# Kernel optimization log

Hardware: AMD Instinct MI355X
Metric: run time of the kernel (lower is better)

The kernel has to match this reference:

```python
import jax, jax.numpy as jnp
import numpy as np

H = 32  # d_model
EPS = 1e-5  # LayerNorm eps (PyTorch default)


def _lstm_layer(x, W_ih, W_hh, b_ih, b_hh):
    """Single LSTM layer, batch_first x: (B, T, D) -> ys: (B, T, H).
    PyTorch gate order: i, f, g, o."""
    B, T, _ = x.shape
    # Hoist the input projection out of the recurrence: one big GEMM.
    xg = jnp.einsum('btd,gd->btg', x, W_ih) + b_ih + b_hh  # (B, T, 4H)
    xg = jnp.swapaxes(xg, 0, 1)  # (T, B, 4H) for scan over time

    def step(carry, xg_t):
        h, c = carry
        gates = xg_t + h @ W_hh.T  # (B, 4H)
        i, f, g, o = jnp.split(gates, 4, axis=-1)
        i = jax.nn.sigmoid(i)
        f = jax.nn.sigmoid(f)
        g = jnp.tanh(g)
        o = jax.nn.sigmoid(o)
        c = f * c + i * g
        h = o * jnp.tanh(c)
        return (h, c), h

    h0 = jnp.zeros((B, H), dtype=x.dtype)
    c0 = jnp.zeros((B, H), dtype=x.dtype)
    (_, _), ys = jax.lax.scan(step, (h0, c0), xg)
    return jnp.swapaxes(ys, 0, 1)  # (B, T, H)


def setup_inputs() -> dict:
    key = jax.random.key(0)
    ks = jax.random.split(key, 10)
    B, T, D = 4096, 512, 6
    s = 1.0 / np.sqrt(H)  # PyTorch LSTM init scale
    inp = {
        'x': jax.random.normal(ks[0], (B, T, D), dtype=jnp.float32),
        # layer 0: input_dim=6 -> H
        'W_ih0': jax.random.uniform(ks[1], (4 * H, D), minval=-s, maxval=s, dtype=jnp.float32),
        'W_hh0': jax.random.uniform(ks[2], (4 * H, H), minval=-s, maxval=s, dtype=jnp.float32),
        'b_ih0': jax.random.uniform(ks[3], (4 * H,), minval=-s, maxval=s, dtype=jnp.float32),
        'b_hh0': jax.random.uniform(ks[4], (4 * H,), minval=-s, maxval=s, dtype=jnp.float32),
        # layer 1: H -> H
        'W_ih1': jax.random.uniform(ks[5], (4 * H, H), minval=-s, maxval=s, dtype=jnp.float32),
        'W_hh1': jax.random.uniform(ks[6], (4 * H, H), minval=-s, maxval=s, dtype=jnp.float32),
        'b_ih1': jax.random.uniform(ks[7], (4 * H,), minval=-s, maxval=s, dtype=jnp.float32),
        'b_hh1': jax.random.uniform(ks[8], (4 * H,), minval=-s, maxval=s, dtype=jnp.float32),
        # final LayerNorm params
        'ln_gamma': jnp.ones((H,), dtype=jnp.float32),
        'ln_beta': jnp.zeros((H,), dtype=jnp.float32),
    }
    return inp


def reference(x, W_ih0, W_hh0, b_ih0, b_hh0, W_ih1, W_hh1, b_ih1, b_hh1, ln_gamma, ln_beta):
    # Two-layer LSTM (dropout between layers is a no-op in eval mode).
    h1 = _lstm_layer(x, W_ih0, W_hh0, b_ih0, b_hh0)   # (B, T, H)
    h2 = _lstm_layer(h1, W_ih1, W_hh1, b_ih1, b_hh1)  # (B, T, H)
    last = h2[:, -1, :]  # (B, H)
    mu = jnp.mean(last, axis=-1, keepdims=True)
    var = jnp.var(last, axis=-1, keepdims=True)
    return (last - mu) / jnp.sqrt(var + EPS) * ln_gamma + ln_beta
```

## Files before the change

kernel.cpp:

```cpp
#include <hip/hip_runtime.h>

#define TT   512
#define DD   6
#define HD   32
#define CH   32
#define EPSL 1e-5f
#define L2E  1.44269504f
#define L2E2 2.88539008f

typedef _Float16 half8 __attribute__((ext_vector_type(8)));
typedef __attribute__((ext_vector_type(4))) float f32x4;

#define MFMA_F16(a, b, c) __builtin_amdgcn_mfma_f32_16x16x32_f16((a), (b), (c), 0, 0, 0)

__global__ __launch_bounds__(256, 1) void lstm2_pipe(
    const float* __restrict__ x,
    const float* __restrict__ W_ih0,
    const float* __restrict__ W_hh0,
    const float* __restrict__ b_ih0,
    const float* __restrict__ b_hh0,
    const float* __restrict__ W_ih1,
    const float* __restrict__ W_hh1,
    const float* __restrict__ b_ih1,
    const float* __restrict__ b_hh1,
    const float* __restrict__ gamma,
    const float* __restrict__ beta,
    float* __restrict__ out)
{
    const int tid = threadIdx.x;
    const int w   = tid >> 6;
    const int L   = w >> 1;
    const int uh  = w & 1;
    const int ln  = tid & 63;
    const int q   = ln >> 4;
    const int n   = ln & 15;
    const int u   = 16 * uh + n;
    const int b0  = blockIdx.x << 4;

    __shared__ __align__(16) _Float16 h0r[4][16][40];
    __shared__ __align__(16) _Float16 h1r[2][16][40];
    __shared__ __align__(16) _Float16 xs[2][CH][16][8];
    __shared__ float ln_s[16][33];

    {
        unsigned* p0 = (unsigned*)&h0r[0][0][0];
        for (int i = tid; i < (int)(sizeof(h0r) / 4); i += 256) p0[i] = 0u;
        unsigned* p1 = (unsigned*)&h1r[0][0][0];
        for (int i = tid; i < (int)(sizeof(h1r) / 4); i += 256) p1[i] = 0u;
        unsigned* p2 = (unsigned*)&xs[0][0][0][0];
        for (int i = tid; i < (int)(sizeof(xs) / 4); i += 256) p2[i] = 0u;
    }
    __syncthreads();

    const float* Wa = L ? W_ih1 : W_hh0;
    const float* bi = L ? b_ih1 : b_ih0;
    const float* bh = L ? b_hh1 : b_hh0;

#define SETUP(p, SC) \
    half8 Ba##p, Bb##p; float K##p; { \
        const int g = 32 * (p) + u; \
        const float4* r4 = (const float4*)(Wa + g * 32 + 8 * q); \
        float4 va = r4[0], vb = r4[1]; \
        Ba##p = half8{(_Float16)(SC * va.x), (_Float16)(SC * va.y), \
                      (_Float16)(SC * va.z), (_Float16)(SC * va.w), \
                      (_Float16)(SC * vb.x), (_Float16)(SC * vb.y), \
                      (_Float16)(SC * vb.z), (_Float16)(SC * vb.w)}; \
        Bb##p = half8{0, 0, 0, 0, 0, 0, 0, 0}; \
        if (L) { \
            const float4* s4 = (const float4*)(W_hh1 + g * 32 + 8 * q); \
            float4 sa = s4[0], sb = s4[1]; \
            Bb##p = half8{(_Float16)(SC * sa.x), (_Float16)(SC * sa.y), \
                          (_Float16)(SC * sa.z), (_Float16)(SC * sa.w), \
                          (_Float16)(SC * sb.x), (_Float16)(SC * sb.y), \
                          (_Float16)(SC * sb.z), (_Float16)(SC * sb.w)}; \
        } else if (q == 0) { \
            const float* xw = W_ih0 + g * 6; \
            Bb##p[0] = (_Float16)(SC * xw[0]); Bb##p[1] = (_Float16)(SC * xw[1]); \
            Bb##p[2] = (_Float16)(SC * xw[2]); Bb##p[3] = (_Float16)(SC * xw[3]); \
            Bb##p[4] = (_Float16)(SC * xw[4]); Bb##p[5] = (_Float16)(SC * xw[5]); \
        } \
        K##p = __builtin_amdgcn_exp2f(SC * (bi[g] + bh[g])); \
    }
    SETUP(0, -L2E) SETUP(1, -L2E) SETUP(2, -L2E2) SETUP(3, -L2E)
    const float K2c = L2E2 * K2;

    const int m0 = (tid       ) / 48, j0 = (tid       ) % 48;
    const int m1 = (tid + 256 ) / 48, j1 = (tid + 256 ) % 48;
    const int m2 = (tid + 512 ) / 48, j2 = (tid + 512 ) % 48;
    float4 xr0, xr1, xr2;

#define XLOAD(ch) { \
        const float* cb = x + (size_t)b0 * (TT * DD) + (ch) * (CH * DD); \
        xr0 = *(const float4*)(cb + (size_t)m0 * (TT * DD) + 4 * j0); \
        xr1 = *(const float4*)(cb + (size_t)m1 * (TT * DD) + 4 * j1); \
        xr2 = *(const float4*)(cb + (size_t)m2 * (TT * DD) + 4 * j2); }

#define XSTORE(buf) { \
        _Float16* xb_ = &xs[(buf)][0][0][0]; \
        { int f = 4 * j0; float4 v = xr0; \
          xb_[((f+0)/6)*128 + m0*8 + ((f+0)%6)] = (_Float16)v.x; \
          xb_[((f+1)/6)*128 + m0*8 + ((f+1)%6)] = (_Float16)v.y; \
          xb_[((f+2)/6)*128 + m0*8 + ((f+2)%6)] = (_Float16)v.z; \
          xb_[((f+3)/6)*128 + m0*8 + ((f+3)%6)] = (_Float16)v.w; } \
        { int f = 4 * j1; float4 v = xr1; \
          xb_[((f+0)/6)*128 + m1*8 + ((f+0)%6)] = (_Float16)v.x; \
          xb_[((f+1)/6)*128 + m1*8 + ((f+1)%6)] = (_Float16)v.y; \
          xb_[((f+2)/6)*128 + m1*8 + ((f+2)%6)] = (_Float16)v.z; \
          xb_[((f+3)/6)*128 + m1*8 + ((f+3)%6)] = (_Float16)v.w; } \
        { int f = 4 * j2; float4 v = xr2; \
          xb_[((f+0)/6)*128 + m2*8 + ((f+0)%6)] = (_Float16)v.x; \
          xb_[((f+1)/6)*128 + m2*8 + ((f+1)%6)] = (_Float16)v.y; \
          xb_[((f+2)/6)*128 + m2*8 + ((f+2)%6)] = (_Float16)v.z; \
          xb_[((f+3)/6)*128 + m2*8 + ((f+3)%6)] = (_Float16)v.w; } }

    XLOAD(0)
    XSTORE(0)

    float cc0 = 0.f, cc1 = 0.f, cc2 = 0.f, cc3 = 0.f;
    float hL0 = 0.f, hL1 = 0.f, hL2 = 0.f, hL3 = 0.f;
    half8 AaN = {0,0,0,0,0,0,0,0};
    half8 AbN = {0,0,0,0,0,0,0,0};
    const f32x4 ZACC = {0.f, 0.f, 0.f, 0.f};

    __syncthreads();

    AbN = *(const half8*)&xs[0][0][n][0];

#define GATE_L0(p) \
    f32x4 acc##p = MFMA_F16(AbN, Bb##p, ZACC); \
    acc##p = MFMA_F16(Aa, Ba##p, acc##p);
#define GATE_L1(p) \
    f32x4 acc##p = MFMA_F16(AaN, Ba##p, ZACC); \
    acc##p = MFMA_F16(Ab, Bb##p, acc##p);

#define UPD(r, IS_L1, WS) { \
        float e0 = __builtin_amdgcn_exp2f(acc0[r]); \
        float e1 = __builtin_amdgcn_exp2f(acc1[r]); \
        float e2 = __builtin_amdgcn_exp2f(acc2[r]); \
        float e3 = __builtin_amdgcn_exp2f(acc3[r]); \
        float pA = fmaf(K0, e0, 1.0f); \
        float pF = fmaf(K1, e1, 1.0f); \
        float pB = fmaf(K2, e2, 1.0f); \
        float pO = fmaf(K3, e3, 1.0f); \
        float Qh = fmaf(K2c, e2, -L2E2); \
        float P  = pA * pB; \
        float R  = __builtin_amdgcn_rcpf(P * pF); \
        float nm = fmaf(cc##r, P, Qh * pF); \
        cc##r = nm * R; \
        float ec = __builtin_amdgcn_exp2f(cc##r); \
        float R2 = __builtin_amdgcn_rcpf(pO * (1.0f + ec)); \
        float h_ = (1.0f - ec) * R2; \
        if (IS_L1) { hL##r = h_; h1r[WS][4 * q + r][u] = (_Float16)h_; } \
        else       {             h0r[WS][4 * q + r][u] = (_Float16)h_; } }

#define BODY(J, S) { \
        if ((J) == 0 && ((S) & (CH - 1)) == 0 && (S) < TT - CH) { XLOAD(((S) >> 5) + 1) } \
        if (L) { \
            half8 Ab      = *(const half8*)&h1r[((J) + 1) & 1][n][8 * q]; \
            half8 AaN_nxt = *(const half8*)&h0r[((J) + 3) & 3][n][8 * q]; \
            if ((S) >= 2 && (S) < TT + 2) { \
                GATE_L1(0) GATE_L1(1) GATE_L1(2) GATE_L1(3) \
                UPD(0, 1, (J) & 1) UPD(1, 1, (J) & 1) \
                UPD(2, 1, (J) & 1) UPD(3, 1, (J) & 1) \
            } \
            AaN = AaN_nxt; \
        } else { \
            half8 Aa      = *(const half8*)&h0r[((J) + 3) & 3][n][8 * q]; \
            const int sn  = ((S) + 1 < TT) ? (S) + 1 : (S); \
            half8 AbN_nxt = *(const half8*)&xs[(sn >> 5) & 1][sn & (CH - 1)][n][0]; \
            if ((S) < TT) { \
                GATE_L0(0) GATE_L0(1) GATE_L0(2) GATE_L0(3) \
                UPD(0, 0, (J) & 3) UPD(1, 0, (J) & 3) \
                UPD(2, 0, (J) & 3) UPD(3, 0, (J) & 3) \
            } \
            AbN = AbN_nxt; \
        } \
        if ((J) == 2 && (((S) & (CH - 1)) == 30) && (S) < TT - 2) { XSTORE((((S) >> 5) + 1) & 1) } \
        __syncthreads(); }

    #pragma unroll 1
    for (int s0 = 0; s0 < 516; s0 += 4) {
        BODY(0, s0)
        BODY(1, s0 + 1)
        BODY(2, s0 + 2)
        BODY(3, s0 + 3)
    }

    if (L) {
        ln_s[4 * q + 0][u] = hL0;
        ln_s[4 * q + 1][u] = hL1;
        ln_s[4 * q + 2][u] = hL2;
        ln_s[4 * q + 3][u] = hL3;
    }
    __syncthreads();

    if (tid < 16) {
        const int m = tid;
        float s = 0.f, s2 = 0.f;
        #pragma unroll
        for (int k = 0; k < HD; ++k) {
            float v = ln_s[m][k];
            s += v; s2 += v * v;
        }
        float mu  = s * (1.0f / HD);
        float var = s2 * (1.0f / HD) - mu * mu;
        float rr  = rsqrtf(var + EPSL);
        float* op = out + (size_t)(b0 + m) * HD;
        #pragma unroll
        for (int k = 0; k < HD; ++k)
            op[k] = (ln_s[m][k] - mu) * rr * gamma[k] + beta[k];
    }
}

extern "C" void kernel_launch(void* const* d_in, const int* in_sizes, int n_in,
                              void* d_out, int out_size, void* d_ws, size_t ws_size,
                              hipStream_t stream) {
    const float* x     = (const float*)d_in[0];
    const float* W_ih0 = (const float*)d_in[1];
    const float* W_hh0 = (const float*)d_in[2];
    const float* b_ih0 = (const float*)d_in[3];
    const float* b_hh0 = (const float*)d_in[4];
    const float* W_ih1 = (const float*)d_in[5];
    const float* W_hh1 = (const float*)d_in[6];
    const float* b_ih1 = (const float*)d_in[7];
    const float* b_hh1 = (const float*)d_in[8];
    const float* gamma = (const float*)d_in[9];
    const float* beta  = (const float*)d_in[10];
    float* out = (float*)d_out;

    const int B = in_sizes[0] / (TT * DD);
    lstm2_pipe<<<B / 16, 256, 0, stream>>>(x, W_ih0, W_hh0, b_ih0, b_hh0,
                                           W_ih1, W_hh1, b_ih1, b_hh1,
                                           gamma, beta, out);
}
```

Measured before the change: 308.5 us.

## Double block to 512 threads, splitting gate updates across wave pairs

Doubles the workgroup to 8 waves so each (layer, unit-half) is handled by two waves. Both waves still issue all four MFMAs, but each applies the elementwise gate update to only two of its four accumulator rows. The intent is to halve the serial transcendental/update work per wave on the recurrence critical path by spreading it across more waves. The cost is duplicated MFMA work, more waves contending for each SIMD, and barriers over twice as many threads. The x-chunk load is also redistributed so that 512 threads cover the 768 float4 loads.

After: 305.8 us. Within noise of the previous version (-0.9%).

```diff
diff --git a/kernel.cpp b/kernel.cpp
--- a/kernel.cpp
+++ b/kernel.cpp
@@ -13,7 +13,7 @@
 
 #define MFMA_F16(a, b, c) __builtin_amdgcn_mfma_f32_16x16x32_f16((a), (b), (c), 0, 0, 0)
 
-__global__ __launch_bounds__(256, 1) void lstm2_pipe(
+__global__ __launch_bounds__(512, 2) void lstm2_pipe(
     const float* __restrict__ x,
     const float* __restrict__ W_ih0,
     const float* __restrict__ W_hh0,
@@ -29,8 +29,9 @@
 {
     const int tid = threadIdx.x;
     const int w   = tid >> 6;
-    const int L   = w >> 1;
-    const int uh  = w & 1;
+    const int L   = w >> 2;
+    const int uh  = (w >> 1) & 1;
+    const int bh  = w & 1;
     const int ln  = tid & 63;
     const int q   = ln >> 4;
     const int n   = ln & 15;
@@ -44,17 +45,17 @@
 
     {
         unsigned* p0 = (unsigned*)&h0r[0][0][0];
-        for (int i = tid; i < (int)(sizeof(h0r) / 4); i += 256) p0[i] = 0u;
+        for (int i = tid; i < (int)(sizeof(h0r) / 4); i += 512) p0[i] = 0u;
         unsigned* p1 = (unsigned*)&h1r[0][0][0];
-        for (int i = tid; i < (int)(sizeof(h1r) / 4); i += 256) p1[i] = 0u;
+        for (int i = tid; i < (int)(sizeof(h1r) / 4); i += 512) p1[i] = 0u;
         unsigned* p2 = (unsigned*)&xs[0][0][0][0];
-        for (int i = tid; i < (int)(sizeof(xs) / 4); i += 256) p2[i] = 0u;
+        for (int i = tid; i < (int)(sizeof(xs) / 4); i += 512) p2[i] = 0u;
     }
     __syncthreads();
 
     const float* Wa = L ? W_ih1 : W_hh0;
     const float* bi = L ? b_ih1 : b_ih0;
-    const float* bh = L ? b_hh1 : b_hh0;
+    const float* bh_ = L ? b_hh1 : b_hh0;
 
 #define SETUP(p, SC) \
     half8 Ba##p, Bb##p; float K##p; { \
@@ -79,39 +80,30 @@
             Bb##p[2] = (_Float16)(SC * xw[2]); Bb##p[3] = (_Float16)(SC * xw[3]); \
             Bb##p[4] = (_Float16)(SC * xw[4]); Bb##p[5] = (_Float16)(SC * xw[5]); \
         } \
-        K##p = __builtin_amdgcn_exp2f(SC * (bi[g] + bh[g])); \
+        K##p = __builtin_amdgcn_exp2f(SC * (bi[g] + bh_[g])); \
     }
     SETUP(0, -L2E) SETUP(1, -L2E) SETUP(2, -L2E2) SETUP(3, -L2E)
     const float K2c = L2E2 * K2;
 
     const int m0 = (tid       ) / 48, j0 = (tid       ) % 48;
     const int m1 = (tid + 256 ) / 48, j1 = (tid + 256 ) % 48;
-    const int m2 = (tid + 512 ) / 48, j2 = (tid + 512 ) % 48;
-    float4 xr0, xr1, xr2;
+    float4 xr0, xr1;
 
 #define XLOAD(ch) { \
         const float* cb = x + (size_t)b0 * (TT * DD) + (ch) * (CH * DD); \
         xr0 = *(const float4*)(cb + (size_t)m0 * (TT * DD) + 4 * j0); \
-        xr1 = *(const float4*)(cb + (size_t)m1 * (TT * DD) + 4 * j1); \
-        xr2 = *(const float4*)(cb + (size_t)m2 * (TT * DD) + 4 * j2); }
+        if (tid >= 256) xr1 = *(const float4*)(cb + (size_t)m1 * (TT * DD) + 4 * j1); }
+
+#define XST1(mm, jj, v) { int f = 4 * (jj); \
+          xb_[((f+0)/6)*128 + (mm)*8 + ((f+0)%6)] = (_Float16)v.x; \
+          xb_[((f+1)/6)*128 + (mm)*8 + ((f+1)%6)] = (_Float16)v.y; \
+          xb_[((f+2)/6)*128 + (mm)*8 + ((f+2)%6)] = (_Float16)v.z; \
+          xb_[((f+3)/6)*128 + (mm)*8 + ((f+3)%6)] = (_Float16)v.w; }
 
 #define XSTORE(buf) { \
         _Float16* xb_ = &xs[(buf)][0][0][0]; \
-        { int f = 4 * j0; float4 v = xr0; \
-          xb_[((f+0)/6)*128 + m0*8 + ((f+0)%6)] = (_Float16)v.x; \
-          xb_[((f+1)/6)*128 + m0*8 + ((f+1)%6)] = (_Float16)v.y; \
-          xb_[((f+2)/6)*128 + m0*8 + ((f+2)%6)] = (_Float16)v.z; \
-          xb_[((f+3)/6)*128 + m0*8 + ((f+3)%6)] = (_Float16)v.w; } \
-        { int f = 4 * j1; float4 v = xr1; \
-          xb_[((f+0)/6)*128 + m1*8 + ((f+0)%6)] = (_Float16)v.x; \
-          xb_[((f+1)/6)*128 + m1*8 + ((f+1)%6)] = (_Float16)v.y; \
-          xb_[((f+2)/6)*128 + m1*8 + ((f+2)%6)] = (_Float16)v.z; \
-          xb_[((f+3)/6)*128 + m1*8 + ((f+3)%6)] = (_Float16)v.w; } \
-        { int f = 4 * j2; float4 v = xr2; \
-          xb_[((f+0)/6)*128 + m2*8 + ((f+0)%6)] = (_Float16)v.x; \
-          xb_[((f+1)/6)*128 + m2*8 + ((f+1)%6)] = (_Float16)v.y; \
-          xb_[((f+2)/6)*128 + m2*8 + ((f+2)%6)] = (_Float16)v.z; \
-          xb_[((f+3)/6)*128 + m2*8 + ((f+3)%6)] = (_Float16)v.w; } }
+        XST1(m0, j0, xr0) \
+        if (tid >= 256) { XST1(m1, j1, xr1) } }
 
     XLOAD(0)
     XSTORE(0)
@@ -160,8 +152,8 @@
             half8 AaN_nxt = *(const half8*)&h0r[((J) + 3) & 3][n][8 * q]; \
             if ((S) >= 2 && (S) < TT + 2) { \
                 GATE_L1(0) GATE_L1(1) GATE_L1(2) GATE_L1(3) \
-                UPD(0, 1, (J) & 1) UPD(1, 1, (J) & 1) \
-                UPD(2, 1, (J) & 1) UPD(3, 1, (J) & 1) \
+                if (bh == 0) { UPD(0, 1, (J) & 1) UPD(1, 1, (J) & 1) } \
+                else         { UPD(2, 1, (J) & 1) UPD(3, 1, (J) & 1) } \
             } \
             AaN = AaN_nxt; \
         } else { \
@@ -170,8 +162,8 @@
             half8 AbN_nxt = *(const half8*)&xs[(sn >> 5) & 1][sn & (CH - 1)][n][0]; \
             if ((S) < TT) { \
                 GATE_L0(0) GATE_L0(1) GATE_L0(2) GATE_L0(3) \
-                UPD(0, 0, (J) & 3) UPD(1, 0, (J) & 3) \
-                UPD(2, 0, (J) & 3) UPD(3, 0, (J) & 3) \
+                if (bh == 0) { UPD(0, 0, (J) & 3) UPD(1, 0, (J) & 3) } \
+                else         { UPD(2, 0, (J) & 3) UPD(3, 0, (J) & 3) } \
             } \
             AbN = AbN_nxt; \
         } \
@@ -187,10 +179,13 @@
     }
 
     if (L) {
-        ln_s[4 * q + 0][u] = hL0;
-        ln_s[4 * q + 1][u] = hL1;
-        ln_s[4 * q + 2][u] = hL2;
-        ln_s[4 * q + 3][u] = hL3;
+        if (bh == 0) {
+            ln_s[4 * q + 0][u] = hL0;
+            ln_s[4 * q + 1][u] = hL1;
+        } else {
+            ln_s[4 * q + 2][u] = hL2;
+            ln_s[4 * q + 3][u] = hL3;
+        }
     }
     __syncthreads();
 
@@ -224,12 +219,12 @@
     const float* W_hh1 = (const float*)d_in[6];
     const float* b_ih1 = (const float*)d_in[7];
     const float* b_hh1 = (const float*)d_in[8];
-    const float* gamma = (const float*)d_in[9];
+    const float* b_    = (const float*)d_in[9];
     const float* beta  = (const float*)d_in[10];
     float* out = (float*)d_out;
 
     const int B = in_sizes[0] / (TT * DD);
-    lstm2_pipe<<<B / 16, 256, 0, stream>>>(x, W_ih0, W_hh0, b_ih0, b_hh0,
+    lstm2_pipe<<<B / 16, 512, 0, stream>>>(x, W_ih0, W_hh0, b_ih0, b_hh0,
                                            W_ih1, W_hh1, b_ih1, b_hh1,
-                                           gamma, beta, out);
+                                           b_, beta, out);
 }
```
